# Performance work log

Measured on AMD Instinct MI355X. Metric: run time of the kernel, lower is better.

Reference implementation:

```python
import jax, jax.numpy as jnp
import numpy as np

B, N, PREV, PRED, H = 16, 64, 6, 30, 256
E = N * (N - 1)
BN_EPS = 1e-5


def _mlp(x, W1, b1, W2, b2, gamma, beta):
    # Two-layer ELU MLP with batch norm over flattened (batch*rows) dim.
    h = jax.nn.elu(x @ W1 + b1)
    h = jax.nn.elu(h @ W2 + b2)
    b, n, d = h.shape
    f = h.reshape(b * n, d)
    mu = f.mean(axis=0)
    var = f.var(axis=0)
    f = (f - mu) * jax.lax.rsqrt(var + BN_EPS) * gamma + beta
    return f.reshape(b, n, d)


def setup_inputs() -> dict:
    key = jax.random.key(0)
    ks = jax.random.split(key, 8)
    # fully-connected directed graph without self loops
    recv, send = np.where(~np.eye(N, dtype=bool))  # each [E]
    rel_rec = jnp.broadcast_to(jax.nn.one_hot(jnp.asarray(recv), N)[None], (B, E, N)).astype(jnp.float32)
    rel_send = jnp.broadcast_to(jax.nn.one_hot(jnp.asarray(send), N)[None], (B, E, N)).astype(jnp.float32)

    def xavier(k, shape):
        fan_in, fan_out = shape
        std = np.sqrt(2.0 / (fan_in + fan_out))
        return jax.random.normal(k, shape, jnp.float32) * std

    return {
        "prev_actor_centers": jax.random.normal(ks[0], (B, N, PREV, 2), jnp.float32) * 10.0,
        "rel_rec": rel_rec,
        "rel_send": rel_send,
        "W_traj": xavier(ks[1], (PREV * 2, H)),
        "b_traj": jnp.full((H,), 0.1, jnp.float32),
        "n2e_W1": xavier(ks[2], (2 * H, H)),
        "n2e_b1": jnp.full((H,), 0.1, jnp.float32),
        "n2e_W2": xavier(ks[3], (H, H)),
        "n2e_b2": jnp.full((H,), 0.1, jnp.float32),
        "n2e_gamma": jnp.ones((H,), jnp.float32),
        "n2e_beta": jnp.zeros((H,), jnp.float32),
        "e2n_W1": xavier(ks[4], (2 * H, H)),
        "e2n_b1": jnp.full((H,), 0.1, jnp.float32),
        "e2n_W2": xavier(ks[5], (H, H)),
        "e2n_b2": jnp.full((H,), 0.1, jnp.float32),
        "e2n_gamma": jnp.ones((H,), jnp.float32),
        "e2n_beta": jnp.zeros((H,), jnp.float32),
        "W_fuse": xavier(ks[6], (2 * H, H)),
        "b_fuse": jnp.full((H,), 0.1, jnp.float32),
        "W_pred": xavier(ks[7], (H, PRED * 2)),
        "b_pred": jnp.full((PRED * 2,), 0.1, jnp.float32),
    }


def reference(prev_actor_centers, rel_rec, rel_send,
              W_traj, b_traj,
              n2e_W1, n2e_b1, n2e_W2, n2e_b2, n2e_gamma, n2e_beta,
              e2n_W1, e2n_b1, e2n_W2, e2n_b2, e2n_gamma, e2n_beta,
              W_fuse, b_fuse, W_pred, b_pred):
    b, n, prev, _ = prev_actor_centers.shape
    # relative displacements, first step zero
    diffs = prev_actor_centers[:, :, 1:, :] - prev_actor_centers[:, :, :-1, :]
    rel_pos = jnp.concatenate([jnp.zeros((b, n, 1, 2), prev_actor_centers.dtype), diffs], axis=2)
    rel_pos = rel_pos.reshape(b, n, prev * 2)
    x = rel_pos @ W_traj + b_traj  # [b, n, H] node features

    # node2edge: gather via one-hot relation matmuls
    receivers = jnp.einsum('ben,bnh->beh', rel_rec, x)
    senders = jnp.einsum('ben,bnh->beh', rel_send, x)
    edges = jnp.concatenate([receivers, senders], axis=-1)  # [b, E, 2H]
    e = _mlp(edges, n2e_W1, n2e_b1, n2e_W2, n2e_b2, n2e_gamma, n2e_beta)

    # edge2node: degree-normalized scatter via transposed relation matmuls
    deg_rec = rel_rec.sum(axis=1)  # [b, n]
    deg_rec = deg_rec + (deg_rec == 0).astype(deg_rec.dtype)
    incoming = jnp.einsum('ben,beh->bnh', rel_rec, e) / deg_rec[..., None]
    deg_send = rel_send.sum(axis=1)
    deg_send = deg_send + (deg_send == 0).astype(deg_send.dtype)
    outgoing = jnp.einsum('ben,beh->bnh', rel_send, e) / deg_send[..., None]
    nodes = jnp.concatenate([incoming, outgoing], axis=-1)  # [b, n, 2H]
    m = _mlp(nodes, e2n_W1, e2n_b1, e2n_W2, e2n_b2, e2n_gamma, e2n_beta)

    fused = jnp.concatenate([x, m], axis=-1) @ W_fuse + b_fuse  # [b, n, H]
    rel = fused @ W_pred + b_pred  # [b, n, PRED*2]

    current_loc = prev_actor_centers[:, :, -1, :]  # [b, n, 2]
    current_loc = jnp.broadcast_to(current_loc[:, :, None, :], (b, n, PRED, 2)).reshape(b, n, PRED * 2)
    pos = jnp.cumsum(rel.reshape(b, n, PRED, 2), axis=2).reshape(b, n, PRED * 2) + current_loc
    return (rel, pos)
```

## Files before the change

kernel.cpp:

```cpp
#include <hip/hip_runtime.h>
#include <hip/hip_bf16.h>

#define BB 16
#define NN 64
#define PREVN 6
#define PREDN 30
#define HH 256
#define EE 4032
#define EROWS (BB*EE)
#define NROWS (BB*NN)

typedef short short8 __attribute__((ext_vector_type(8)));
typedef float f32x4 __attribute__((ext_vector_type(4)));

enum : int {
  OFF_STATS_E = 0,
  OFF_STATS_M = 1024,
  OFF_XRS     = 2048,
  F32_END     = 264192
};
enum : size_t {
  BO_W1TE  = 0,
  BO_W2TE  = 131072,
  BO_W1TN  = 196608,
  BO_W2TN  = 327680,
  BO_WFT   = 393216,
  BO_WPT   = 524288,
  BO_XG    = 540672,
  BO_NODES = 802816,
  BO_H1G   = 1327104,
  BO_M2    = 1589248,
  BO_FG    = 1851392,
  BO_E2    = 2113536
};

__device__ __forceinline__ float eluf(float v) { return v > 0.f ? v : __expf(v) - 1.f; }

__device__ __forceinline__ float xembed(const float* __restrict__ centers,
                                        const float* __restrict__ Wt,
                                        const float* __restrict__ bt,
                                        int rr, int col) {
  const float* c = centers + rr * 12;
  float acc = bt[col];
  #pragma unroll
  for (int t = 0; t < 5; ++t) {
    float dx = c[(t+1)*2 + 0] - c[t*2 + 0];
    float dy = c[(t+1)*2 + 1] - c[t*2 + 1];
    acc += dx * Wt[(2 + 2*t)*HH + col] + dy * Wt[(3 + 2*t)*HH + col];
  }
  return acc;
}

struct PrepArgs {
  const float *centers, *W_traj, *b_traj;
  const float *n2e_W1, *n2e_W2, *e2n_W1, *e2n_W2, *W_fuse, *W_pred;
  float* ws;
  float* inc;
  __hip_bfloat16 *w1te, *w2te, *w1tn, *w2tn, *wft, *wpt, *xg;
};

__global__ __launch_bounds__(256) void k_prep(PrepArgs a) {
  __shared__ float t[64][65];
  const int bid = blockIdx.x, tid = threadIdx.x;
  if (bid < 128) {
    const float* W; __hip_bfloat16* WT; int K, lb;
    if (bid < 32)      { W = a.n2e_W1; WT = a.w1te; K = 512; lb = bid; }
    else if (bid < 48) { W = a.n2e_W2; WT = a.w2te; K = 256; lb = bid - 32; }
    else if (bid < 80) { W = a.e2n_W1; WT = a.w1tn; K = 512; lb = bid - 48; }
    else if (bid < 96) { W = a.e2n_W2; WT = a.w2tn; K = 256; lb = bid - 80; }
    else               { W = a.W_fuse; WT = a.wft;  K = 512; lb = bid - 96; }
    int KB = K / 64;
    int k0 = (lb % KB) * 64, n0 = (lb / KB) * 64;
    int tx = tid & 63, ty = tid >> 6;
    #pragma unroll
    for (int i = 0; i < 16; ++i)
      t[ty + i*4][tx] = W[(size_t)(k0 + ty + i*4) * 256 + n0 + tx];
    __syncthreads();
    #pragma unroll
    for (int i = 0; i < 16; ++i)
      WT[(size_t)(n0 + ty + i*4) * K + k0 + tx] = __float2bfloat16(t[tx][ty + i*4]);
  } else if (bid < 192) {
    int idx = (bid - 128) * 256 + tid;
    int c = idx >> 8, k = idx & 255;
    a.wpt[idx] = __float2bfloat16(c < 60 ? a.W_pred[k * 60 + c] : 0.f);
  } else if (bid < 200) {
    a.ws[(bid - 192) * 256 + tid] = 0.f;
  } else if (bid < 264) {
    int row0 = (bid - 200) * 16;
    #pragma unroll
    for (int r = 0; r < 16; ++r)
      a.xg[(size_t)(row0 + r)*256 + tid] =
          __float2bfloat16(xembed(a.centers, a.W_traj, a.b_traj, row0 + r, tid));
  } else {
    float* p = a.inc + (size_t)(bid - 264) * 4096;
    #pragma unroll
    for (int i = 0; i < 4; ++i)
      *reinterpret_cast<float4*>(p + (i*256 + tid)*4) = (float4){0.f,0.f,0.f,0.f};
  }
}

__global__ __launch_bounds__(64) void k_xrs2(
    const __hip_bfloat16* __restrict__ xg,
    const __hip_bfloat16* __restrict__ W1T,
    const float* __restrict__ b1,
    __hip_bfloat16* __restrict__ xrs) {
  const int lane = threadIdx.x;
  const int m16 = lane & 15, quad = lane >> 4;
  const int ko = quad * 8;
  const int rt = blockIdx.x >> 3, s = blockIdx.x & 7;
  const int half = s >> 2, j0 = (s & 3) * 64;
  const int row0 = rt * 16;
  __hip_bfloat16* dst = xrs + (size_t)half * 262144;

  f32x4 acc[4];
  #pragma unroll
  for (int jt = 0; jt < 4; ++jt) {
    float bv = half ? 0.f : b1[j0 + jt*16 + m16];
    acc[jt] = (f32x4){bv, bv, bv, bv};
  }
  #pragma unroll
  for (int ks = 0; ks < 8; ++ks) {
    short8 af = *reinterpret_cast<const short8*>(
        xg + (size_t)(row0 + m16)*256 + ks*32 + ko);
    short8 bf[4];
    #pragma unroll
    for (int jt = 0; jt < 4; ++jt)
      bf[jt] = *reinterpret_cast<const short8*>(
          W1T + (size_t)(j0 + jt*16 + m16)*512 + half*256 + ks*32 + ko);
    #pragma unroll
    for (int jt = 0; jt < 4; ++jt)
      acc[jt] = __builtin_amdgcn_mfma_f32_16x16x32_bf16(af, bf[jt], acc[jt], 0, 0, 0);
  }
  #pragma unroll
  for (int jt = 0; jt < 4; ++jt)
    #pragma unroll
    for (int r = 0; r < 4; ++r)
      dst[(size_t)(row0 + quad*4 + r)*256 + j0 + jt*16 + m16] =
          __float2bfloat16(acc[jt][r]);
}

__global__ __launch_bounds__(256, 4) void k_mlp7(
    const __hip_bfloat16* __restrict__ xrs,
    const __hip_bfloat16* __restrict__ W2T,
    const float* __restrict__ b2,
    __hip_bfloat16* __restrict__ outp,
    float* __restrict__ stats,
    float* __restrict__ incraw) {
  __shared__ alignas(16) __hip_bfloat16 h1s[64][264];
  __shared__ float sst[3][256];
  const int tid = threadIdx.x;
  const int w = tid >> 6, lane = tid & 63;
  const int m16 = lane & 15, quad = lane >> 4;
  const int ko = quad * 8;
  const int blk = blockIdx.x;
  const int bb = blk / 63, lb = blk - bb*63;
  const int row0 = blk * 64;
  const int n0 = (lb * 64) / 63;
  const int thr = (n0 + 1) * 63 - lb * 64;
  const int colw = w * 64;

  #pragma unroll
  for (int i = 0; i < 3; ++i) sst[i][tid] = 0.f;

  {
    const int rg = tid >> 5;
    const int c8 = (tid & 31) * 8;
    const __hip_bfloat16* xrb = xrs + (size_t)(bb*64 + n0)*256 + c8;
    const __hip_bfloat16* xsb = xrs + 262144 + (size_t)bb*64*256 + c8;
    union { uint4 u; __hip_bfloat16 h[8]; } vr0, vr1;
    vr0.u = *reinterpret_cast<const uint4*>(xrb);
    vr1.u = *reinterpret_cast<const uint4*>(xrb + 256);
    #pragma unroll
    for (int i = 0; i < 8; ++i) {
      int r = rg + i*8;
      int isn1 = (r >= thr) ? 1 : 0;
      int rc = n0 + isn1;
      int jj = lb*64 + r - rc*63;
      int sd = jj + (jj >= rc ? 1 : 0);
      union { uint4 u; __hip_bfloat16 h[8]; } vs, va, o;
      vs.u = *reinterpret_cast<const uint4*>(xsb + (size_t)sd*256);
      va.u = isn1 ? vr1.u : vr0.u;
      #pragma unroll
      for (int j = 0; j < 8; ++j)
        o.h[j] = __float2bfloat16(eluf(__bfloat162float(va.h[j]) +
                                       __bfloat162float(vs.h[j])));
      *reinterpret_cast<uint4*>(&h1s[r][c8]) = o.u;
    }
  }
  __syncthreads();

  f32x4 acc2[4][4];
  #pragma unroll
  for (int jt = 0; jt < 4; ++jt) {
    float bv = b2[colw + jt*16 + m16];
    #pragma unroll
    for (int mt = 0; mt < 4; ++mt) acc2[mt][jt] = (f32x4){bv, bv, bv, bv};
  }
  #pragma unroll
  for (int kt = 0; kt < 4; ++kt) {
    #pragma unroll
    for (int ks = 0; ks < 2; ++ks) {
      const int k0 = kt*64 + ks*32 + ko;
      short8 af[4], bf[4];
      #pragma unroll
      for (int jt = 0; jt < 4; ++jt)
        bf[jt] = *reinterpret_cast<const short8*>(
            W2T + (size_t)(colw + jt*16 + m16)*256 + k0);
      #pragma unroll
      for (int mt = 0; mt < 4; ++mt)
        af[mt] = *(const short8*)((const char*)h1s +
                     (size_t)(mt*16 + m16)*528 + k0*2);
      #pragma unroll
      for (int mt = 0; mt < 4; ++mt)
        #pragma unroll
        for (int jt = 0; jt < 4; ++jt)
          acc2[mt][jt] = __builtin_amdgcn_mfma_f32_16x16x32_bf16(af[mt], bf[jt],
                                                                 acc2[mt][jt], 0, 0, 0);
    }
  }
  __syncthreads();

  #pragma unroll
  for (int jt = 0; jt < 4; ++jt) {
    float s0 = 0.f, s1 = 0.f, sq = 0.f;
    #pragma unroll
    for (int mt = 0; mt < 4; ++mt)
      #pragma unroll
      for (int r = 0; r < 4; ++r) {
        int row = mt*16 + quad*4 + r;
        float hv = eluf(acc2[mt][jt][r]);
        h1s[row][colw + jt*16 + m16] = __float2bfloat16(hv);
        float t1 = (row >= thr) ? hv : 0.f;
        s1 += t1; s0 += hv - t1;
        sq += hv * hv;
      }
    atomicAdd(&sst[0][colw + jt*16 + m16], s0);
    atomicAdd(&sst[1][colw + jt*16 + m16], s1);
    atomicAdd(&sst[2][colw + jt*16 + m16], sq);
  }
  __syncthreads();

  {
    float s0 = sst[0][tid], s1 = sst[1][tid];
    atomicAdd(&stats[tid], s0 + s1);
    atomicAdd(&stats[256 + tid], sst[2][tid]);
    atomicAdd(&incraw[(size_t)(bb*64 + n0)*256 + tid], s0);
    atomicAdd(&incraw[(size_t)(bb*64 + n0 + 1)*256 + tid], s1);
  }
  #pragma unroll
  for (int i = 0; i < 8; ++i) {
    int u = i*256 + tid;
    int r = u >> 5, c = (u & 31) * 8;
    *reinterpret_cast<uint4*>(outp + (size_t)(row0 + r)*HH + c) =
        *reinterpret_cast<const uint4*>(&h1s[r][c]);
  }
}

__global__ __launch_bounds__(256) void k_aggS(const __hip_bfloat16* __restrict__ e2,
                                              const float* __restrict__ incraw,
                                              const float* __restrict__ st,
                                              const float* __restrict__ gam,
                                              const float* __restrict__ bet,
                                              __hip_bfloat16* __restrict__ nodes) {
  __shared__ float red[8][256];
  const int bn = blockIdx.x;
  const int b = bn >> 6, n = bn & 63;
  const int tid = threadIdx.x;
  const int c8 = (tid & 31) * 8;
  const int rg = tid >> 5;
  const __hip_bfloat16* base = e2 + (size_t)b * EE * HH;
  float s[8] = {0.f,0.f,0.f,0.f,0.f,0.f,0.f,0.f};
  for (int j = rg; j < 63; j += 8) {
    int i = j + (j >= n ? 1 : 0);
    int e = i*63 + n - (n > i ? 1 : 0);
    union { uint4 u; __hip_bfloat16 h[8]; } v;
    v.u = *reinterpret_cast<const uint4*>(base + (size_t)e*HH + c8);
    #pragma unroll
    for (int jj = 0; jj < 8; ++jj) s[jj] += __bfloat162float(v.h[jj]);
  }
  #pragma unroll
  for (int jj = 0; jj < 8; jj += 4)
    *reinterpret_cast<float4*>(&red[rg][c8 + jj]) =
        (float4){s[jj], s[jj+1], s[jj+2], s[jj+3]};
  __syncthreads();
  float S = 0.f;
  #pragma unroll
  for (int r = 0; r < 8; ++r) S += red[r][tid];
  const float inv = 1.f / (float)EROWS;
  float mean = st[tid] * inv;
  float var  = fmaxf(st[256 + tid] * inv - mean*mean, 0.f);
  float a = gam[tid] * rsqrtf(var + 1e-5f);
  float c0 = bet[tid] - mean * a;
  float in_v  = a * (incraw[(size_t)bn*256 + tid] * (1.f/63.f)) + c0;
  float out_v = a * (S * (1.f/63.f)) + c0;
  nodes[(size_t)bn*512 + tid]       = __float2bfloat16(in_v);
  nodes[(size_t)bn*512 + 256 + tid] = __float2bfloat16(out_v);
}

__global__ __launch_bounds__(64) void k_n1(
    const __hip_bfloat16* __restrict__ nodes,
    const __hip_bfloat16* __restrict__ W1T,
    const float* __restrict__ b1,
    __hip_bfloat16* __restrict__ h1g) {
  __shared__ alignas(16) __hip_bfloat16 hls[16][40];
  const int lane = threadIdx.x;
  const int m16 = lane & 15, quad = lane >> 4;
  const int ko = quad * 8;
  const int row0 = (blockIdx.x >> 3) * 16;
  const int j0 = (blockIdx.x & 7) * 32;

  f32x4 acc[2];
  #pragma unroll
  for (int jt = 0; jt < 2; ++jt) {
    float bv = b1[j0 + jt*16 + m16];
    acc[jt] = (f32x4){bv, bv, bv, bv};
  }
  #pragma unroll
  for (int ks = 0; ks < 16; ++ks) {
    short8 af = *reinterpret_cast<const short8*>(
        nodes + (size_t)(row0 + m16)*512 + ks*32 + ko);
    short8 bf[2];
    #pragma unroll
    for (int jt = 0; jt < 2; ++jt)
      bf[jt] = *reinterpret_cast<const short8*>(
          W1T + (size_t)(j0 + jt*16 + m16)*512 + ks*32 + ko);
    #pragma unroll
    for (int jt = 0; jt < 2; ++jt)
      acc[jt] = __builtin_amdgcn_mfma_f32_16x16x32_bf16(af, bf[jt], acc[jt], 0, 0, 0);
  }
  #pragma unroll
  for (int jt = 0; jt < 2; ++jt)
    #pragma unroll
    for (int r = 0; r < 4; ++r)
      hls[quad*4 + r][jt*16 + m16] = __float2bfloat16(eluf(acc[jt][r]));
  {
    int r = lane >> 2, c = (lane & 3) * 8;
    *reinterpret_cast<uint4*>(h1g + (size_t)(row0 + r)*256 + j0 + c) =
        *reinterpret_cast<const uint4*>(&hls[r][c]);
  }
}

__global__ __launch_bounds__(64) void k_n2(
    const __hip_bfloat16* __restrict__ h1g,
    const __hip_bfloat16* __restrict__ W2T,
    const float* __restrict__ b2,
    __hip_bfloat16* __restrict__ m2,
    float* __restrict__ stats) {
  __shared__ alignas(16) __hip_bfloat16 hls[16][40];
  __shared__ float sst[2][32];
  const int lane = threadIdx.x;
  const int m16 = lane & 15, quad = lane >> 4;
  const int ko = quad * 8;
  const int row0 = (blockIdx.x >> 3) * 16;
  const int j0 = (blockIdx.x & 7) * 32;

  if (lane < 32) { sst[0][lane] = 0.f; sst[1][lane] = 0.f; }

  f32x4 acc[2];
  #pragma unroll
  for (int jt = 0; jt < 2; ++jt) {
    float bv = b2[j0 + jt*16 + m16];
    acc[jt] = (f32x4){bv, bv, bv, bv};
  }
  #pragma unroll
  for (int ks = 0; ks < 8; ++ks) {
    short8 af = *reinterpret_cast<const short8*>(
        h1g + (size_t)(row0 + m16)*256 + ks*32 + ko);
    short8 bf[2];
    #pragma unroll
    for (int jt = 0; jt < 2; ++jt)
      bf[jt] = *reinterpret_cast<const short8*>(
          W2T + (size_t)(j0 + jt*16 + m16)*256 + ks*32 + ko);
    #pragma unroll
    for (int jt = 0; jt < 2; ++jt)
      acc[jt] = __builtin_amdgcn_mfma_f32_16x16x32_bf16(af, bf[jt], acc[jt], 0, 0, 0);
  }
  #pragma unroll
  for (int jt = 0; jt < 2; ++jt) {
    float ps = 0.f, pq = 0.f;
    #pragma unroll
    for (int r = 0; r < 4; ++r) {
      float hv = eluf(acc[jt][r]);
      hls[quad*4 + r][jt*16 + m16] = __float2bfloat16(hv);
      ps += hv; pq += hv * hv;
    }
    atomicAdd(&sst[0][jt*16 + m16], ps);
    atomicAdd(&sst[1][jt*16 + m16], pq);
  }
  if (lane < 32) {
    atomicAdd(&stats[j0 + lane], sst[0][lane]);
    atomicAdd(&stats[256 + j0 + lane], sst[1][lane]);
  }
  {
    int r = lane >> 2, c = (lane & 3) * 8;
    *reinterpret_cast<uint4*>(m2 + (size_t)(row0 + r)*256 + j0 + c) =
        *reinterpret_cast<const uint4*>(&hls[r][c]);
  }
}

__global__ __launch_bounds__(64) void k_hf(
    const __hip_bfloat16* __restrict__ xg,
    const __hip_bfloat16* __restrict__ m2,
    const float* __restrict__ stM,
    const float* __restrict__ gam,
    const float* __restrict__ bet,
    const __hip_bfloat16* __restrict__ WfT,
    const float* __restrict__ bfv,
    __hip_bfloat16* __restrict__ fg) {
  __shared__ alignas(16) __hip_bfloat16 hls[16][40];
  __shared__ float bnA[256], bnC[256];
  const int lane = threadIdx.x;
  const int m16 = lane & 15, quad = lane >> 4;
  const int ko = quad * 8;
  const int row0 = (blockIdx.x >> 3) * 16;
  const int j0 = (blockIdx.x & 7) * 32;

  {
    const float inv = 1.f / (float)NROWS;
    #pragma unroll
    for (int j = 0; j < 4; ++j) {
      int k = lane*4 + j;
      float mean = stM[k] * inv;
      float var  = fmaxf(stM[256 + k] * inv - mean*mean, 0.f);
      float am = gam[k] * rsqrtf(var + 1e-5f);
      bnA[k] = am;
      bnC[k] = bet[k] - mean * am;
    }
  }

  f32x4 acc[2];
  #pragma unroll
  for (int jt = 0; jt < 2; ++jt) {
    float bv = bfv[j0 + jt*16 + m16];
    acc[jt] = (f32x4){bv, bv, bv, bv};
  }
  #pragma unroll
  for (int ks = 0; ks < 16; ++ks) {
    short8 af;
    if (ks < 8) {
      af = *reinterpret_cast<const short8*>(
          xg + (size_t)(row0 + m16)*256 + ks*32 + ko);
    } else {
      int k0 = (ks - 8)*32 + ko;
      union { uint4 u; __hip_bfloat16 h[8]; } v;
      v.u = *reinterpret_cast<const uint4*>(m2 + (size_t)(row0 + m16)*256 + k0);
      union { short8 s8; __hip_bfloat16 h[8]; } o;
      #pragma unroll
      for (int j = 0; j < 8; ++j)
        o.h[j] = __float2bfloat16(bnA[k0+j] * __bfloat162float(v.h[j]) + bnC[k0+j]);
      af = o.s8;
    }
    short8 bf[2];
    #pragma unroll
    for (int jt = 0; jt < 2; ++jt)
      bf[jt] = *reinterpret_cast<const short8*>(
          WfT + (size_t)(j0 + jt*16 + m16)*512 + ks*32 + ko);
    #pragma unroll
    for (int jt = 0; jt < 2; ++jt)
      acc[jt] = __builtin_amdgcn_mfma_f32_16x16x32_bf16(af, bf[jt], acc[jt], 0, 0, 0);
  }
  #pragma unroll
  for (int jt = 0; jt < 2; ++jt)
    #pragma unroll
    for (int r = 0; r < 4; ++r)
      hls[quad*4 + r][jt*16 + m16] = __float2bfloat16(acc[jt][r]);
  {
    int r = lane >> 2, c = (lane & 3) * 8;
    *reinterpret_cast<uint4*>(fg + (size_t)(row0 + r)*256 + j0 + c) =
        *reinterpret_cast<const uint4*>(&hls[r][c]);
  }
}

__global__ __launch_bounds__(64) void k_pred(
    const __hip_bfloat16* __restrict__ fg,
    const __hip_bfloat16* __restrict__ WpT,
    const float* __restrict__ bp,
    const float* __restrict__ centers,
    float* __restrict__ out) {
  __shared__ float rl[16][68];
  const int lane = threadIdx.x;
  const int m16 = lane & 15, quad = lane >> 4;
  const int ko = quad * 8;
  const int row0 = blockIdx.x * 16;

  f32x4 acc[4];
  #pragma unroll
  for (int jt = 0; jt < 4; ++jt) {
    int c = jt*16 + m16;
    float bv = (c < 60) ? bp[c] : 0.f;
    acc[jt] = (f32x4){bv, bv, bv, bv};
  }
  #pragma unroll
  for (int ks = 0; ks < 8; ++ks) {
    short8 af = *reinterpret_cast<const short8*>(
        fg + (size_t)(row0 + m16)*256 + ks*32 + ko);
    short8 bf[4];
    #pragma unroll
    for (int jt = 0; jt < 4; ++jt)
      bf[jt] = *reinterpret_cast<const short8*>(
          WpT + (size_t)(jt*16 + m16)*256 + ks*32 + ko);
    #pragma unroll
    for (int jt = 0; jt < 4; ++jt)
      acc[jt] = __builtin_amdgcn_mfma_f32_16x16x32_bf16(af, bf[jt], acc[jt], 0, 0, 0);
  }
  #pragma unroll
  for (int jt = 0; jt < 4; ++jt) {
    int c = jt*16 + m16;
    #pragma unroll
    for (int r = 0; r < 4; ++r) {
      int lr = quad*4 + r;
      rl[lr][c] = acc[jt][r];
      if (c < 60) out[(size_t)(row0 + lr)*60 + c] = acc[jt][r];
    }
  }
  if (lane < 32) {
    int lr = lane >> 1, xy = lane & 1;
    int grow = row0 + lr;
    float run = centers[(size_t)(grow*PREVN + 5)*2 + xy];
    #pragma unroll
    for (int p = 0; p < PREDN; ++p) {
      run += rl[lr][2*p + xy];
      out[61440 + (size_t)grow*60 + 2*p + xy] = run;
    }
  }
}

extern "C" void kernel_launch(void* const* d_in, const int* in_sizes, int n_in,
                              void* d_out, int out_size, void* d_ws, size_t ws_size,
                              hipStream_t stream) {
  const float* centers = (const float*)d_in[0];
  float* ws = (float*)d_ws;
  __hip_bfloat16* wb = (__hip_bfloat16*)(ws + F32_END);
  __hip_bfloat16* xrs = (__hip_bfloat16*)(ws + OFF_XRS);
  float* incraw = (float*)(wb + BO_H1G);

  const float* W_traj = (const float*)d_in[3];
  const float* b_traj = (const float*)d_in[4];
  const float* n2e_b1 = (const float*)d_in[6];
  const float* n2e_b2 = (const float*)d_in[8];
  const float* n2e_g  = (const float*)d_in[9];
  const float* n2e_be = (const float*)d_in[10];
  const float* e2n_b1 = (const float*)d_in[12];
  const float* e2n_b2 = (const float*)d_in[14];
  const float* e2n_g  = (const float*)d_in[15];
  const float* e2n_be = (const float*)d_in[16];
  const float* b_fuse = (const float*)d_in[18];
  const float* b_pred = (const float*)d_in[20];

  PrepArgs pa;
  pa.centers = centers; pa.W_traj = W_traj; pa.b_traj = b_traj;
  pa.n2e_W1 = (const float*)d_in[5];  pa.n2e_W2 = (const float*)d_in[7];
  pa.e2n_W1 = (const float*)d_in[11]; pa.e2n_W2 = (const float*)d_in[13];
  pa.W_fuse = (const float*)d_in[17]; pa.W_pred = (const float*)d_in[19];
  pa.ws = ws; pa.inc = incraw;
  pa.w1te = wb + BO_W1TE; pa.w2te = wb + BO_W2TE;
  pa.w1tn = wb + BO_W1TN; pa.w2tn = wb + BO_W2TN;
  pa.wft = wb + BO_WFT;   pa.wpt = wb + BO_WPT;
  pa.xg = wb + BO_XG;

  k_prep<<<328, 256, 0, stream>>>(pa);
  k_xrs2<<<512, 64, 0, stream>>>(wb + BO_XG, wb + BO_W1TE, n2e_b1, xrs);
  k_mlp7<<<EROWS/64, 256, 0, stream>>>(xrs, wb + BO_W2TE, n2e_b2, wb + BO_E2,
                                       ws + OFF_STATS_E, incraw);
  k_aggS<<<NROWS, 256, 0, stream>>>(wb + BO_E2, incraw, ws + OFF_STATS_E,
                                    n2e_g, n2e_be, wb + BO_NODES);
  k_n1<<<512, 64, 0, stream>>>(wb + BO_NODES, wb + BO_W1TN, e2n_b1, wb + BO_H1G);
  k_n2<<<512, 64, 0, stream>>>(wb + BO_H1G, wb + BO_W2TN, e2n_b2, wb + BO_M2,
                               ws + OFF_STATS_M);
  k_hf<<<512, 64, 0, stream>>>(wb + BO_XG, wb + BO_M2, ws + OFF_STATS_M,
                               e2n_g, e2n_be, wb + BO_WFT, b_fuse, wb + BO_FG);
  k_pred<<<64, 64, 0, stream>>>(wb + BO_FG, wb + BO_WPT, b_pred, centers,
                                (float*)d_out);
}
```

Baseline: 201.8 us.

## Pre-pack weights in MFMA fragment order and store edges grouped by sender

The prep kernel now writes each weight matrix in the exact per-lane MFMA B-fragment order, so every GEMM kernel loads its B operand as one contiguous 16-byte chunk per lane instead of strided transposed rows. The edge MLP also scatters its output rows into a sender-major layout, which lets the outgoing aggregation kernel read 63 contiguous rows per node instead of gathering scattered edge indices. In exchange, the prep kernel does strided fp32 reads with scalar bf16 writes, and the edge-output stores from the MLP become scattered rather than contiguous.

```diff
diff --git a/kernel.cpp b/kernel.cpp
--- a/kernel.cpp
+++ b/kernel.cpp
@@ -56,43 +56,46 @@
   const float *n2e_W1, *n2e_W2, *e2n_W1, *e2n_W2, *W_fuse, *W_pred;
   float* ws;
   float* inc;
-  __hip_bfloat16 *w1te, *w2te, *w1tn, *w2tn, *wft, *wpt, *xg;
+  __hip_bfloat16 *p1e, *p2e, *p1n, *p2n, *pf, *pp, *xg;
 };
 
 __global__ __launch_bounds__(256) void k_prep(PrepArgs a) {
-  __shared__ float t[64][65];
   const int bid = blockIdx.x, tid = threadIdx.x;
-  if (bid < 128) {
-    const float* W; __hip_bfloat16* WT; int K, lb;
-    if (bid < 32)      { W = a.n2e_W1; WT = a.w1te; K = 512; lb = bid; }
-    else if (bid < 48) { W = a.n2e_W2; WT = a.w2te; K = 256; lb = bid - 32; }
-    else if (bid < 80) { W = a.e2n_W1; WT = a.w1tn; K = 512; lb = bid - 48; }
-    else if (bid < 96) { W = a.e2n_W2; WT = a.w2tn; K = 256; lb = bid - 80; }
-    else               { W = a.W_fuse; WT = a.wft;  K = 512; lb = bid - 96; }
-    int KB = K / 64;
-    int k0 = (lb % KB) * 64, n0 = (lb / KB) * 64;
-    int tx = tid & 63, ty = tid >> 6;
-    #pragma unroll
-    for (int i = 0; i < 16; ++i)
-      t[ty + i*4][tx] = W[(size_t)(k0 + ty + i*4) * 256 + n0 + tx];
-    __syncthreads();
-    #pragma unroll
-    for (int i = 0; i < 16; ++i)
-      WT[(size_t)(n0 + ty + i*4) * K + k0 + tx] = __float2bfloat16(t[tx][ty + i*4]);
-  } else if (bid < 192) {
-    int idx = (bid - 128) * 256 + tid;
-    int c = idx >> 8, k = idx & 255;
-    a.wpt[idx] = __float2bfloat16(c < 60 ? a.W_pred[k * 60 + c] : 0.f);
-  } else if (bid < 200) {
-    a.ws[(bid - 192) * 256 + tid] = 0.f;
-  } else if (bid < 264) {
-    int row0 = (bid - 200) * 16;
+  if (bid < 264) {
+    const float* W; __hip_bfloat16* P; int ksh, t0, pad = 0;
+    if (bid < 64)       { W = a.n2e_W1; P = a.p1e; ksh = 4; t0 = bid*4; }
+    else if (bid < 96)  { W = a.n2e_W2; P = a.p2e; ksh = 3; t0 = (bid-64)*4; }
+    else if (bid < 160) { W = a.e2n_W1; P = a.p1n; ksh = 4; t0 = (bid-96)*4; }
+    else if (bid < 192) { W = a.e2n_W2; P = a.p2n; ksh = 3; t0 = (bid-160)*4; }
+    else if (bid < 256) { W = a.W_fuse; P = a.pf;  ksh = 4; t0 = (bid-192)*4; }
+    else                { W = a.W_pred; P = a.pp;  ksh = 3; t0 = (bid-256)*4; pad = 1; }
+    const int l = tid & 63, sub = tid >> 6;
+    const int t = t0 + sub;
+    const int j = t >> ksh, ks = t & ((1 << ksh) - 1);
+    const int m16 = l & 15, q = l >> 4;
+    __hip_bfloat16* dst = P + ((size_t)t*64 + l)*8;
+    if (!pad) {
+      const float* src = W + (size_t)(ks*32 + q*8)*256 + j*16 + m16;
+      #pragma unroll
+      for (int e = 0; e < 8; ++e)
+        dst[e] = __float2bfloat16(src[(size_t)e*256]);
+    } else {
+      const int col = j*16 + m16;
+      #pragma unroll
+      for (int e = 0; e < 8; ++e)
+        dst[e] = __float2bfloat16(col < 60 ?
+                     W[(size_t)(ks*32 + q*8 + e)*60 + col] : 0.f);
+    }
+  } else if (bid < 272) {
+    a.ws[(bid - 264) * 256 + tid] = 0.f;
+  } else if (bid < 336) {
+    int row0 = (bid - 272) * 16;
     #pragma unroll
     for (int r = 0; r < 16; ++r)
       a.xg[(size_t)(row0 + r)*256 + tid] =
           __float2bfloat16(xembed(a.centers, a.W_traj, a.b_traj, row0 + r, tid));
   } else {
-    float* p = a.inc + (size_t)(bid - 264) * 4096;
+    float* p = a.inc + (size_t)(bid - 336) * 4096;
     #pragma unroll
     for (int i = 0; i < 4; ++i)
       *reinterpret_cast<float4*>(p + (i*256 + tid)*4) = (float4){0.f,0.f,0.f,0.f};
@@ -101,7 +104,7 @@
 
 __global__ __launch_bounds__(64) void k_xrs2(
     const __hip_bfloat16* __restrict__ xg,
-    const __hip_bfloat16* __restrict__ W1T,
+    const __hip_bfloat16* __restrict__ W1P,
     const float* __restrict__ b1,
     __hip_bfloat16* __restrict__ xrs) {
   const int lane = threadIdx.x;
@@ -109,6 +112,7 @@
   const int ko = quad * 8;
   const int rt = blockIdx.x >> 3, s = blockIdx.x & 7;
   const int half = s >> 2, j0 = (s & 3) * 64;
+  const int jg0 = (s & 3) * 4;
   const int row0 = rt * 16;
   __hip_bfloat16* dst = xrs + (size_t)half * 262144;
 
@@ -126,7 +130,7 @@
     #pragma unroll
     for (int jt = 0; jt < 4; ++jt)
       bf[jt] = *reinterpret_cast<const short8*>(
-          W1T + (size_t)(j0 + jt*16 + m16)*512 + half*256 + ks*32 + ko);
+          W1P + (((size_t)(jg0 + jt)*16 + half*8 + ks)*64 + lane)*8);
     #pragma unroll
     for (int jt = 0; jt < 4; ++jt)
       acc[jt] = __builtin_amdgcn_mfma_f32_16x16x32_bf16(af, bf[jt], acc[jt], 0, 0, 0);
@@ -139,9 +143,9 @@
           __float2bfloat16(acc[jt][r]);
 }
 
-__global__ __launch_bounds__(256, 4) void k_mlp7(
+__global__ __launch_bounds__(256, 4) void k_mlp8(
     const __hip_bfloat16* __restrict__ xrs,
-    const __hip_bfloat16* __restrict__ W2T,
+    const __hip_bfloat16* __restrict__ W2P,
     const float* __restrict__ b2,
     __hip_bfloat16* __restrict__ outp,
     float* __restrict__ stats,
@@ -154,7 +158,6 @@
   const int ko = quad * 8;
   const int blk = blockIdx.x;
   const int bb = blk / 63, lb = blk - bb*63;
-  const int row0 = blk * 64;
   const int n0 = (lb * 64) / 63;
   const int thr = (n0 + 1) * 63 - lb * 64;
   const int colw = w * 64;
@@ -201,11 +204,12 @@
     #pragma unroll
     for (int ks = 0; ks < 2; ++ks) {
       const int k0 = kt*64 + ks*32 + ko;
+      const int chunk = kt*2 + ks;
       short8 af[4], bf[4];
       #pragma unroll
       for (int jt = 0; jt < 4; ++jt)
         bf[jt] = *reinterpret_cast<const short8*>(
-            W2T + (size_t)(colw + jt*16 + m16)*256 + k0);
+            W2P + (((size_t)(w*4 + jt)*8 + chunk)*64 + lane)*8);
       #pragma unroll
       for (int mt = 0; mt < 4; ++mt)
         af[mt] = *(const short8*)((const char*)h1s +
@@ -251,7 +255,12 @@
   for (int i = 0; i < 8; ++i) {
     int u = i*256 + tid;
     int r = u >> 5, c = (u & 31) * 8;
-    *reinterpret_cast<uint4*>(outp + (size_t)(row0 + r)*HH + c) =
+    int isn1 = (r >= thr) ? 1 : 0;
+    int rc = n0 + isn1;
+    int jj = lb*64 + r - rc*63;
+    int sd = jj + (jj >= rc ? 1 : 0);
+    int jpos = rc - (jj < rc ? 1 : 0);
+    *reinterpret_cast<uint4*>(outp + ((size_t)(bb*64 + sd)*63 + jpos)*HH + c) =
         *reinterpret_cast<const uint4*>(&h1s[r][c]);
   }
 }
@@ -264,17 +273,14 @@
                                               __hip_bfloat16* __restrict__ nodes) {
   __shared__ float red[8][256];
   const int bn = blockIdx.x;
-  const int b = bn >> 6, n = bn & 63;
   const int tid = threadIdx.x;
   const int c8 = (tid & 31) * 8;
   const int rg = tid >> 5;
-  const __hip_bfloat16* base = e2 + (size_t)b * EE * HH;
+  const __hip_bfloat16* base = e2 + (size_t)bn * 63 * HH;
   float s[8] = {0.f,0.f,0.f,0.f,0.f,0.f,0.f,0.f};
   for (int j = rg; j < 63; j += 8) {
-    int i = j + (j >= n ? 1 : 0);
-    int e = i*63 + n - (n > i ? 1 : 0);
     union { uint4 u; __hip_bfloat16 h[8]; } v;
-    v.u = *reinterpret_cast<const uint4*>(base + (size_t)e*HH + c8);
+    v.u = *reinterpret_cast<const uint4*>(base + (size_t)j*HH + c8);
     #pragma unroll
     for (int jj = 0; jj < 8; ++jj) s[jj] += __bfloat162float(v.h[jj]);
   }
@@ -299,7 +305,7 @@
 
 __global__ __launch_bounds__(64) void k_n1(
     const __hip_bfloat16* __restrict__ nodes,
-    const __hip_bfloat16* __restrict__ W1T,
+    const __hip_bfloat16* __restrict__ W1P,
     const float* __restrict__ b1,
     __hip_bfloat16* __restrict__ h1g) {
   __shared__ alignas(16) __hip_bfloat16 hls[16][40];
@@ -307,7 +313,8 @@
   const int m16 = lane & 15, quad = lane >> 4;
   const int ko = quad * 8;
   const int row0 = (blockIdx.x >> 3) * 16;
-  const int j0 = (blockIdx.x & 7) * 32;
+  const int jb = blockIdx.x & 7;
+  const int j0 = jb * 32;
 
   f32x4 acc[2];
   #pragma unroll
@@ -323,7 +330,7 @@
     #pragma unroll
     for (int jt = 0; jt < 2; ++jt)
       bf[jt] = *reinterpret_cast<const short8*>(
-          W1T + (size_t)(j0 + jt*16 + m16)*512 + ks*32 + ko);
+          W1P + (((size_t)(jb*2 + jt)*16 + ks)*64 + lane)*8);
     #pragma unroll
     for (int jt = 0; jt < 2; ++jt)
       acc[jt] = __builtin_amdgcn_mfma_f32_16x16x32_bf16(af, bf[jt], acc[jt], 0, 0, 0);
@@ -342,7 +349,7 @@
 
 __global__ __launch_bounds__(64) void k_n2(
     const __hip_bfloat16* __restrict__ h1g,
-    const __hip_bfloat16* __restrict__ W2T,
+    const __hip_bfloat16* __restrict__ W2P,
     const float* __restrict__ b2,
     __hip_bfloat16* __restrict__ m2,
     float* __restrict__ stats) {
@@ -352,7 +359,8 @@
   const int m16 = lane & 15, quad = lane >> 4;
   const int ko = quad * 8;
   const int row0 = (blockIdx.x >> 3) * 16;
-  const int j0 = (blockIdx.x & 7) * 32;
+  const int jb = blockIdx.x & 7;
+  const int j0 = jb * 32;
 
   if (lane < 32) { sst[0][lane] = 0.f; sst[1][lane] = 0.f; }
 
@@ -370,7 +378,7 @@
     #pragma unroll
     for (int jt = 0; jt < 2; ++jt)
       bf[jt] = *reinterpret_cast<const short8*>(
-          W2T + (size_t)(j0 + jt*16 + m16)*256 + ks*32 + ko);
+          W2P + (((size_t)(jb*2 + jt)*8 + ks)*64 + lane)*8);
     #pragma unroll
     for (int jt = 0; jt < 2; ++jt)
       acc[jt] = __builtin_amdgcn_mfma_f32_16x16x32_bf16(af, bf[jt], acc[jt], 0, 0, 0);
@@ -404,7 +412,7 @@
     const float* __restrict__ stM,
     const float* __restrict__ gam,
     const float* __restrict__ bet,
-    const __hip_bfloat16* __restrict__ WfT,
+    const __hip_bfloat16* __restrict__ WfP,
     const float* __restrict__ bfv,
     __hip_bfloat16* __restrict__ fg) {
   __shared__ alignas(16) __hip_bfloat16 hls[16][40];
@@ -413,7 +421,8 @@
   const int m16 = lane & 15, quad = lane >> 4;
   const int ko = quad * 8;
   const int row0 = (blockIdx.x >> 3) * 16;
-  const int j0 = (blockIdx.x & 7) * 32;
+  const int jb = blockIdx.x & 7;
+  const int j0 = jb * 32;
 
   {
     const float inv = 1.f / (float)NROWS;
@@ -454,7 +463,7 @@
     #pragma unroll
     for (int jt = 0; jt < 2; ++jt)
       bf[jt] = *reinterpret_cast<const short8*>(
-          WfT + (size_t)(j0 + jt*16 + m16)*512 + ks*32 + ko);
+          WfP + (((size_t)(jb*2 + jt)*16 + ks)*64 + lane)*8);
     #pragma unroll
     for (int jt = 0; jt < 2; ++jt)
       acc[jt] = __builtin_amdgcn_mfma_f32_16x16x32_bf16(af, bf[jt], acc[jt], 0, 0, 0);
@@ -473,7 +482,7 @@
 
 __global__ __launch_bounds__(64) void k_pred(
     const __hip_bfloat16* __restrict__ fg,
-    const __hip_bfloat16* __restrict__ WpT,
+    const __hip_bfloat16* __restrict__ WpP,
     const float* __restrict__ bp,
     const float* __restrict__ centers,
     float* __restrict__ out) {
@@ -498,7 +507,7 @@
     #pragma unroll
     for (int jt = 0; jt < 4; ++jt)
       bf[jt] = *reinterpret_cast<const short8*>(
-          WpT + (size_t)(jt*16 + m16)*256 + ks*32 + ko);
+          WpP + (((size_t)jt*8 + ks)*64 + lane)*8);
     #pragma unroll
     for (int jt = 0; jt < 4; ++jt)
       acc[jt] = __builtin_amdgcn_mfma_f32_16x16x32_bf16(af, bf[jt], acc[jt], 0, 0, 0);
@@ -553,14 +562,14 @@
   pa.e2n_W1 = (const float*)d_in[11]; pa.e2n_W2 = (const float*)d_in[13];
   pa.W_fuse = (const float*)d_in[17]; pa.W_pred = (const float*)d_in[19];
   pa.ws = ws; pa.inc = incraw;
-  pa.w1te = wb + BO_W1TE; pa.w2te = wb + BO_W2TE;
-  pa.w1tn = wb + BO_W1TN; pa.w2tn = wb + BO_W2TN;
-  pa.wft = wb + BO_WFT;   pa.wpt = wb + BO_WPT;
+  pa.p1e = wb + BO_W1TE; pa.p2e = wb + BO_W2TE;
+  pa.p1n = wb + BO_W1TN; pa.p2n = wb + BO_W2TN;
+  pa.pf = wb + BO_WFT;   pa.pp = wb + BO_WPT;
   pa.xg = wb + BO_XG;
 
-  k_prep<<<328, 256, 0, stream>>>(pa);
+  k_prep<<<400, 256, 0, stream>>>(pa);
   k_xrs2<<<512, 64, 0, stream>>>(wb + BO_XG, wb + BO_W1TE, n2e_b1, xrs);
-  k_mlp7<<<EROWS/64, 256, 0, stream>>>(xrs, wb + BO_W2TE, n2e_b2, wb + BO_E2,
+  k_mlp8<<<EROWS/64, 256, 0, stream>>>(xrs, wb + BO_W2TE, n2e_b2, wb + BO_E2,
                                        ws + OFF_STATS_E, incraw);
   k_aggS<<<NROWS, 256, 0, stream>>>(wb + BO_E2, incraw, ws + OFF_STATS_E,
                                     n2e_g, n2e_be, wb + BO_NODES);
```

Measured after the change: 195.2 us. 1.03x faster.
